# Optimization experiments

Measured on AMD Instinct MI355X. Metric: run time of the kernel, lower is better.

The kernel has to match this reference:

```python
import jax, jax.numpy as jnp
import numpy as np

B, NQ, NK = 4, 2048, 2048
DQ = DK = DV = 512
H = 8
DS = DV // H  # 64


def _layernorm(x, g, b, eps=1e-5):
    m = jnp.mean(x, axis=-1, keepdims=True)
    v = jnp.var(x, axis=-1, keepdims=True)
    return (x - m) * jax.lax.rsqrt(v + eps) * g + b


def setup_inputs() -> dict:
    key = jax.random.key(0)
    ks = jax.random.split(key, 16)
    def lin(k, fan_in, fan_out):
        # torch nn.Linear default init: U(-1/sqrt(fan_in), 1/sqrt(fan_in))
        bound = 1.0 / np.sqrt(fan_in)
        k1, k2 = jax.random.split(k)
        W = jax.random.uniform(k1, (fan_in, fan_out), jnp.float32, -bound, bound)
        b = jax.random.uniform(k2, (fan_out,), jnp.float32, -bound, bound)
        return W, b
    Wq, bq = lin(ks[0], DQ, DV)
    Wk, bk = lin(ks[1], DK, DV)
    Wv, bv = lin(ks[2], DK, DV)
    W0, b0 = lin(ks[3], DV, DV)
    W1, b1 = lin(ks[4], DV, DV)
    # xavier_uniform for kp/vp of shape (1, DS): bound = sqrt(6/(1+DS))
    xb = np.sqrt(6.0 / (1 + DS))
    kp = jax.random.uniform(ks[5], (DS,), jnp.float32, -xb, xb)
    vp = jax.random.uniform(ks[6], (DS,), jnp.float32, -xb, xb)
    return {
        "Q": jax.random.normal(ks[7], (B, NQ, DQ), jnp.float32),
        "K": jax.random.normal(ks[8], (B, NK, DK), jnp.float32),
        "Kpos": jax.random.uniform(ks[9], (B, NQ, NK), jnp.float32),
        "Wq": Wq, "bq": bq, "Wk": Wk, "bk": bk, "Wv": Wv, "bv": bv,
        "kp": kp, "vp": vp,
        "W0": W0, "b0": b0, "W1": W1, "b1": b1,
        "g0": jnp.ones((DV,), jnp.float32), "be0": jnp.zeros((DV,), jnp.float32),
        "g1": jnp.ones((DV,), jnp.float32), "be1": jnp.zeros((DV,), jnp.float32),
    }


def reference(Q, K, Kpos, Wq, bq, Wk, bk, Wv, bv, kp, vp, W0, b0, W1, b1, g0, be0, g1, be1):
    Qp = Q @ Wq + bq                       # [B,NQ,DV]
    Kp = K @ Wk + bk                       # [B,NK,DV]
    Vp = K @ Wv + bv                       # [B,NK,DV]
    # head split (torch split/cat along batch == reshape to [B,N,H,DS])
    Qh = Qp.reshape(B, NQ, H, DS)
    Kh = Kp.reshape(B, NK, H, DS)
    Vh = Vp.reshape(B, NK, H, DS)
    scale = 1.0 / np.sqrt(DV)              # NOTE: original scales by sqrt(dim_V), not per-head dim
    scores = jnp.einsum('bqhd,bkhd->bhqk', Qh, Kh) * scale
    # ShawRE key bias: KE[b,h,q,k] = Kpos[b,q,k] * <Qh[b,q,h,:], kp>
    qkp = jnp.einsum('bqhd,d->bhq', Qh, kp)          # [B,H,NQ]
    scores = scores + Kpos[:, None, :, :] * qkp[:, :, :, None]
    A = jax.nn.softmax(scores, axis=-1)              # [B,H,NQ,NK]
    out = jnp.einsum('bhqk,bkhd->bqhd', A, Vh)       # [B,NQ,H,DS]
    # ShawRE value bias: VE[b,q,h,:] = (sum_k A*Kpos) * vp
    akp = jnp.einsum('bhqk,bqk->bhq', A, Kpos)       # [B,H,NQ]
    out = out + akp.transpose(0, 2, 1)[..., None] * vp
    O = (Qh + out).reshape(B, NQ, DV)
    O = _layernorm(O, g0, be0)
    resO = O
    O = jax.nn.relu(O @ W0 + b0)           # fc_o[0] with relu (numlayers=2)
    O = resO + jax.nn.relu(O @ W1 + b1)    # fc_o[-1] + residual
    O = _layernorm(O, g1, be1)
    return O
```

## Files before the change

### kernel.cpp

```cpp
#include <hip/hip_runtime.h>
#include <math.h>

#define Bx  4
#define NQx 2048
#define NKx 2048
#define Dx  512
#define Hx  8

typedef __attribute__((ext_vector_type(8))) __bf16 bf16x8;
typedef __attribute__((ext_vector_type(4))) float f32x4;
typedef __attribute__((ext_vector_type(16))) float f32x16;

typedef const __attribute__((address_space(1))) unsigned int* gas_ptr;
typedef __attribute__((address_space(3))) unsigned int* lds_ptr;

__device__ __forceinline__ void gload16(const void* g, void* l){
  __builtin_amdgcn_global_load_lds((gas_ptr)g, (lds_ptr)l, 16, 0, 0);
}

__device__ __forceinline__ unsigned short f2bf(float f){
  union { float f; unsigned int u; } v; v.f = f;
  unsigned int r = (v.u + 0x7FFFu + ((v.u >> 16) & 1u)) >> 16;
  return (unsigned short)r;
}
__device__ __forceinline__ float bf2f(unsigned short u){
  union { unsigned int u; float f; } v; v.u = ((unsigned int)u) << 16; return v.f;
}
__device__ __forceinline__ unsigned int cvtpk_bf16(float a, float b){
  unsigned int d;
  asm("v_cvt_pk_bf16_f32 %0, %1, %2" : "=v"(d) : "v"(a), "v"(b));
  return d;
}
__device__ __forceinline__ void plane32_swap(unsigned int& a, unsigned int& b){
  asm("v_permlane32_swap_b32 %0, %1" : "+v"(a), "+v"(b));
}
__device__ __forceinline__ float fexp2(float x){
  float d; asm("v_exp_f32 %0, %1" : "=v"(d) : "v"(x)); return d;
}
__device__ __forceinline__ float fmax3(float a, float b, float c){
  float d; asm("v_max3_f32 %0, %1, %2, %3" : "=v"(d) : "v"(a), "v"(b), "v"(c)); return d;
}

__global__ __launch_bounds__(256) void mab_wt(
    const float* __restrict__ Wq, const float* __restrict__ Wk, const float* __restrict__ Wv,
    const float* __restrict__ W0, const float* __restrict__ W1,
    unsigned short* __restrict__ Wt)
{
  __shared__ unsigned short T[64][72];
  const int z = blockIdx.z;
  const float* W = (z==0)?Wq:(z==1)?Wk:(z==2)?Wv:(z==3)?W0:W1;
  unsigned short* O = Wt + (size_t)z*512*512;
  const int k0 = blockIdx.x*64, n0 = blockIdx.y*64;
  const int tid = threadIdx.x;
  #pragma unroll
  for (int i=0;i<4;++i){
    int id = tid + i*256;
    int r = id>>4, c4 = id&15;
    float4 v = *(const float4*)(W + (size_t)(k0+r)*512 + n0 + c4*4);
    ushort4 o; o.x=f2bf(v.x); o.y=f2bf(v.y); o.z=f2bf(v.z); o.w=f2bf(v.w);
    *(ushort4*)&T[r][c4*4] = o;
  }
  __syncthreads();
  #pragma unroll
  for (int i=0;i<2;++i){
    int id = tid + i*256;
    int c = id>>3, r8 = id&7;
    union { unsigned short u[8]; uint4 v; } o;
    #pragma unroll
    for (int j=0;j<8;++j) o.u[j] = T[r8*8+j][c];
    *(uint4*)(O + (size_t)(n0+c)*512 + k0 + r8*8) = o.v;
  }
}

__global__ __launch_bounds__(256) void mab_vt(
    const unsigned short* __restrict__ Vp, unsigned short* __restrict__ Vpt)
{
  __shared__ unsigned short T[64][72];
  const int r0 = blockIdx.x*64;
  const int c0 = blockIdx.y*64;
  const int b  = blockIdx.z;
  const int tid = threadIdx.x;
  #pragma unroll
  for (int i=0;i<2;++i){
    int id = tid + i*256;
    int r = id>>3, c8 = id&7;
    *(uint4*)&T[r][c8*8] = *(const uint4*)(Vp + (size_t)(b*NKx + r0+r)*512 + c0 + c8*8);
  }
  __syncthreads();
  #pragma unroll
  for (int i=0;i<2;++i){
    int id = tid + i*256;
    int c = id>>3, r8 = id&7;
    union { unsigned short u[8]; uint4 v; } o;
    #pragma unroll
    for (int j=0;j<8;++j) o.u[j] = T[r8*8+j][c];
    *(uint4*)(Vpt + ((size_t)(b*512) + c0 + c)*NKx + r0 + r8*8) = o.v;
  }
}

__global__ __launch_bounds__(256) void mab_gemm_proj(
    const float* __restrict__ Qf, const float* __restrict__ Kf,
    const unsigned short* __restrict__ Wt,
    const float* __restrict__ bq, const float* __restrict__ bk, const float* __restrict__ bv,
    unsigned short* __restrict__ Cb, float kscale)
{
  __shared__ unsigned short As[128][64];
  __shared__ unsigned short Bs[128][64];
  const int z = blockIdx.z;
  const float* A = (z==0) ? Qf : Kf;
  const unsigned short* W = Wt + (size_t)z*512*512;
  const float* bias = (z==0)?bq:((z==1)?bk:bv);
  const float sc = (z==1) ? kscale : 1.0f;
  const int m0 = blockIdx.y*128, n0 = blockIdx.x*128;
  const int tid = threadIdx.x, w = tid>>6, lane = tid&63, g = lane>>4, q16 = lane&15;
  const int wr = w>>1, wc = w&1;

  f32x4 acc[4][4];
  #pragma unroll
  for (int m=0;m<4;++m)
    #pragma unroll
    for (int n=0;n<4;++n) acc[m][n] = (f32x4){0.f,0.f,0.f,0.f};

  float4 areg[8];
  #pragma unroll
  for (int i=0;i<8;++i){
    int id = i*256 + tid, row = id>>4, qc = id&15;
    areg[i] = *(const float4*)(A + (size_t)(m0+row)*512 + qc*4);
  }

  for (int k0 = 0; k0 < 512; k0 += 64){
    __syncthreads();
    #pragma unroll
    for (int i=0;i<8;++i){
      int id = i*256 + tid, row = id>>4, qc = id&15;
      unsigned int lo = cvtpk_bf16(areg[i].x, areg[i].y);
      unsigned int hi = cvtpk_bf16(areg[i].z, areg[i].w);
      unsigned int* dst = (unsigned int*)((char*)&As[0][0] + row*128
                          + ((qc>>1) ^ (row&7))*16 + (qc&1)*8);
      dst[0] = lo; dst[1] = hi;
    }
    #pragma unroll
    for (int i=0;i<4;++i){
      int o   = (w*4 + i)*1024 + lane*16;
      int row = o >> 7;
      int c   = (o >> 4) & 7;
      int cs  = c ^ (row & 7);
      gload16(W + (size_t)(n0+row)*512 + k0 + cs*8, (char*)&Bs[0][0] + (w*4+i)*1024);
    }
    __syncthreads();
    if (k0 + 64 < 512){
      #pragma unroll
      for (int i=0;i<8;++i){
        int id = i*256 + tid, row = id>>4, qc = id&15;
        areg[i] = *(const float4*)(A + (size_t)(m0+row)*512 + (k0+64) + qc*4);
      }
    }
    #pragma unroll
    for (int ks=0;ks<2;++ks){
      bf16x8 af[4], bfr[4];
      #pragma unroll
      for (int m=0;m<4;++m){
        int row = wr*64 + m*16 + q16;
        int c   = (ks*4 + g) ^ (row & 7);
        af[m] = *(const bf16x8*)((const char*)&As[0][0] + row*128 + c*16);
      }
      #pragma unroll
      for (int n=0;n<4;++n){
        int row = wc*64 + n*16 + q16;
        int c   = (ks*4 + g) ^ (row & 7);
        bfr[n] = *(const bf16x8*)((const char*)&Bs[0][0] + row*128 + c*16);
      }
      #pragma unroll
      for (int m=0;m<4;++m)
        #pragma unroll
        for (int n=0;n<4;++n)
          acc[m][n] = __builtin_amdgcn_mfma_f32_16x16x32_bf16(af[m], bfr[n], acc[m][n], 0,0,0);
    }
  }

  const size_t ZS = (size_t)8192*512;
  #pragma unroll
  for (int m=0;m<4;++m){
    const int rowl = wr*64 + m*16 + g*4;
    #pragma unroll
    for (int n=0;n<4;++n){
      const int col = n0 + wc*64 + n*16 + q16;
      const float bv2 = bias[col];
      #pragma unroll
      for (int r=0;r<4;++r){
        float v = (acc[m][n][r] + bv2) * sc;
        Cb[(size_t)z*ZS + (size_t)(m0 + rowl + r)*512 + col] = f2bf(v);
      }
    }
  }
}

__global__ __launch_bounds__(256) void mab_gemm_mfma(
    const unsigned short* __restrict__ A, const unsigned short* __restrict__ W,
    const float* __restrict__ bias, const unsigned short* __restrict__ resb,
    unsigned short* __restrict__ Cb, float* __restrict__ Cf, int relu)
{
  __shared__ unsigned short As[128][64];
  __shared__ unsigned short Bs[128][64];
  const int m0 = blockIdx.y*128, n0 = blockIdx.x*128;
  const int tid = threadIdx.x, w = tid>>6, lane = tid&63, g = lane>>4, q16 = lane&15;
  const int wr = w>>1, wc = w&1;

  f32x4 acc[4][4];
  #pragma unroll
  for (int m=0;m<4;++m)
    #pragma unroll
    for (int n=0;n<4;++n) acc[m][n] = (f32x4){0.f,0.f,0.f,0.f};

  for (int k0 = 0; k0 < 512; k0 += 64){
    __syncthreads();
    #pragma unroll
    for (int i=0;i<4;++i){
      int o   = (w*4 + i)*1024 + lane*16;
      int row = o >> 7;
      int c   = (o >> 4) & 7;
      int cs  = c ^ (row & 7);
      gload16(A + (size_t)(m0+row)*512 + k0 + cs*8, (char*)&As[0][0] + (w*4+i)*1024);
      gload16(W + (size_t)(n0+row)*512 + k0 + cs*8, (char*)&Bs[0][0] + (w*4+i)*1024);
    }
    __syncthreads();
    #pragma unroll
    for (int ks=0;ks<2;++ks){
      bf16x8 af[4], bfr[4];
      #pragma unroll
      for (int m=0;m<4;++m){
        int row = wr*64 + m*16 + q16;
        int c   = (ks*4 + g) ^ (row & 7);
        af[m] = *(const bf16x8*)((const char*)&As[0][0] + row*128 + c*16);
      }
      #pragma unroll
      for (int n=0;n<4;++n){
        int row = wc*64 + n*16 + q16;
        int c   = (ks*4 + g) ^ (row & 7);
        bfr[n] = *(const bf16x8*)((const char*)&Bs[0][0] + row*128 + c*16);
      }
      #pragma unroll
      for (int m=0;m<4;++m)
        #pragma unroll
        for (int n=0;n<4;++n)
          acc[m][n] = __builtin_amdgcn_mfma_f32_16x16x32_bf16(af[m], bfr[n], acc[m][n], 0,0,0);
    }
  }

  #pragma unroll
  for (int m=0;m<4;++m){
    const int rowl = wr*64 + m*16 + g*4;
    #pragma unroll
    for (int n=0;n<4;++n){
      const int col = n0 + wc*64 + n*16 + q16;
      const float bv = bias[col];
      #pragma unroll
      for (int r=0;r<4;++r){
        float v = acc[m][n][r] + bv;
        if (relu) v = fmaxf(v, 0.f);
        size_t off = (size_t)(m0 + rowl + r)*512 + col;
        if (resb) v += bf2f(resb[off]);
        if (Cb) Cb[off] = f2bf(v);
        if (Cf) Cf[off] = v;
      }
    }
  }
}

__global__ __launch_bounds__(512, 2) void mab_attn7(
    const unsigned short* __restrict__ Qp, const unsigned short* __restrict__ Kp,
    const unsigned short* __restrict__ Vpt,
    const float* __restrict__ Kpos, const float* __restrict__ kp, const float* __restrict__ vp,
    float* __restrict__ X)
{
  __shared__ __align__(16) char pool[139264];

  const int qt = blockIdx.x;
  const int b  = blockIdx.y;
  const int q0 = qt*32;
  const int tid = threadIdx.x, w = tid>>6, lane = tid&63;
  const int q32 = lane & 31, hi = lane >> 5;
  const int h = w;

  char* Kbase = pool + w*8192;
  char* Vbase = pool + 65536 + w*8192;
  char* KQb   = pool + 131072;

  const unsigned short* Kg = Kp + ((size_t)b*NKx)*Dx + h*64;
  const unsigned short* Vg = Vpt + ((size_t)(b*512) + h*64)*NKx;
  const float* KPg = Kpos + (size_t)b*NQx*NKx + (size_t)q0*NKx;

  const int sr8 = lane>>3, sc8 = lane&7;
  const int sr4 = lane>>2, sc4 = lane&3;

  #pragma unroll
  for (int i=0;i<4;++i){
    int kr = i*8 + sr8, kcs = sc8 ^ (kr & 7);
    gload16(Kg + (size_t)kr*Dx + kcs*8, Kbase + i*1024);
    int vr = i*16 + sr4, vcs = sc4 ^ ((vr>>1) & 3);
    gload16(Vg + (size_t)vr*NKx + vcs*8, Vbase + i*1024);
  }
  if (w < 4){
    int pr = w*8 + sr8, pcs = sc8 ^ (pr & 7);
    gload16(KPg + (size_t)pr*NKx + pcs*4, KQb + w*1024);
  }

  const unsigned short* Qrowp = Qp + ((size_t)(b*NQx + q0 + q32))*Dx + h*64;
  bf16x8 qf[4];
  #pragma unroll
  for (int ds=0; ds<4; ++ds)
    qf[ds] = *(const bf16x8*)(Qrowp + ds*16 + hi*8);

  float qkp = 0.f;
  #pragma unroll
  for (int ds=0; ds<4; ++ds){
    union { bf16x8 v; unsigned short u[8]; } qa; qa.v = qf[ds];
    #pragma unroll
    for (int j=0;j<8;++j)
      qkp = fmaf(bf2f(qa.u[j]), kp[ds*16 + hi*8 + j], qkp);
  }
  qkp += __shfl_xor(qkp, 32);
  qkp *= 1.4426950408889634f;

  float m_i = -1e30f, l_i = 0.f, a_i = 0.f;
  f32x16 accT[2];
  #pragma unroll
  for (int db=0; db<2; ++db)
    #pragma unroll
    for (int r=0;r<16;++r) accT[db][r] = 0.f;

  __syncthreads();

  for (int t = 0; t < 64; ++t){
    const int cur = t & 1;
    const int k0 = t*32;

    if (t+1 < 64){
      const int k1 = k0 + 32;
      #pragma unroll
      for (int i=0;i<4;++i){
        int kr = i*8 + sr8, kcs = sc8 ^ (kr & 7);
        gload16(Kg + (size_t)(k1 + kr)*Dx + kcs*8, Kbase + (cur^1)*4096 + i*1024);
        int vr = i*16 + sr4, vcs = sc4 ^ ((vr>>1) & 3);
        gload16(Vg + (size_t)vr*NKx + k1 + vcs*8, Vbase + (cur^1)*4096 + i*1024);
      }
      if (w < 4){
        int pr = w*8 + sr8, pcs = sc8 ^ (pr & 7);
        gload16(KPg + (size_t)pr*NKx + k1 + pcs*4, KQb + (cur^1)*4096 + w*1024);
      }
    }
    __builtin_amdgcn_sched_barrier(0);

    f32x16 sT;
    #pragma unroll
    for (int r=0;r<16;++r) sT[r] = 0.f;
    __builtin_amdgcn_s_setprio(1);
    #pragma unroll
    for (int ds=0; ds<4; ++ds){
      int cc = (ds*2 + hi) ^ (q32 & 7);
      bf16x8 kf = *(const bf16x8*)(Kbase + cur*4096 + q32*128 + cc*16);
      sT = __builtin_amdgcn_mfma_f32_32x32x16_bf16(kf, qf[ds], sT, 0,0,0);
    }
    __builtin_amdgcn_s_setprio(0);

    f32x4 kq[4];
    #pragma unroll
    for (int a=0;a<4;++a){
      int cc = (a*2 + hi) ^ (q32 & 7);
      kq[a] = *(const f32x4*)(KQb + cur*4096 + q32*128 + cc*16);
    }

    #pragma unroll
    for (int r=0;r<16;++r)
      sT[r] = fmaf(kq[r>>2][r&3], qkp, sT[r]);

    float t0 = fmax3(sT[0],  sT[1],  sT[2]);
    float t1 = fmax3(sT[3],  sT[4],  sT[5]);
    float t2 = fmax3(sT[6],  sT[7],  sT[8]);
    float t3 = fmax3(sT[9],  sT[10], sT[11]);
    float t4 = fmax3(sT[12], sT[13], sT[14]);
    float rm = fmax3(fmax3(t0, t1, t2), fmax3(t3, t4, sT[15]), m_i);
    rm = fmaxf(rm, __shfl_xor(rm, 32));

    if (!__all(rm <= m_i + 11.544f)){
      float al = fexp2(m_i - rm);
      m_i = rm;
      l_i *= al; a_i *= al;
      #pragma unroll
      for (int db=0; db<2; ++db)
        #pragma unroll
        for (int r=0;r<16;++r) accT[db][r] *= al;
    }

    float psq[4] = {0.f,0.f,0.f,0.f};
    float pkq[4] = {0.f,0.f,0.f,0.f};
    #pragma unroll
    for (int r=0;r<16;++r){
      float p = fexp2(sT[r] - m_i);
      sT[r] = p;
      psq[r&3] += p;
      pkq[r&3] = fmaf(p, kq[r>>2][r&3], pkq[r&3]);
    }
    float ps = (psq[0]+psq[1]) + (psq[2]+psq[3]);
    float pk = (pkq[0]+pkq[1]) + (pkq[2]+pkq[3]);
    ps += __shfl_xor(ps, 32);
    pk += __shfl_xor(pk, 32);
    l_i += ps; a_i += pk;

    union PW { unsigned int u[4]; bf16x8 v; } pa[2];
    {
      unsigned int w0 = cvtpk_bf16(sT[0],  sT[1]);
      unsigned int w1 = cvtpk_bf16(sT[2],  sT[3]);
      unsigned int w2 = cvtpk_bf16(sT[4],  sT[5]);
      unsigned int w3 = cvtpk_bf16(sT[6],  sT[7]);
      unsigned int w4 = cvtpk_bf16(sT[8],  sT[9]);
      unsigned int w5 = cvtpk_bf16(sT[10], sT[11]);
      unsigned int w6 = cvtpk_bf16(sT[12], sT[13]);
      unsigned int w7 = cvtpk_bf16(sT[14], sT[15]);
      plane32_swap(w0, w2);
      plane32_swap(w1, w3);
      plane32_swap(w4, w6);
      plane32_swap(w5, w7);
      pa[0].u[0]=w0; pa[0].u[1]=w1; pa[0].u[2]=w2; pa[0].u[3]=w3;
      pa[1].u[0]=w4; pa[1].u[1]=w5; pa[1].u[2]=w6; pa[1].u[3]=w7;
    }

    __builtin_amdgcn_s_setprio(1);
    #pragma unroll
    for (int c2=0; c2<2; ++c2){
      #pragma unroll
      for (int db=0; db<2; ++db){
        int row = db*32 + q32;
        int cc  = (c2*2 + hi) ^ ((row>>1) & 3);
        bf16x8 vf = *(const bf16x8*)(Vbase + cur*4096 + row*64 + cc*16);
        accT[db] = __builtin_amdgcn_mfma_f32_32x32x16_bf16(vf, pa[c2].v, accT[db], 0,0,0);
      }
    }
    __builtin_amdgcn_s_setprio(0);

    __syncthreads();
  }

  float inv = 1.0f / l_i;
  float aw  = a_i * inv;
  float* Xrow = X + ((size_t)(b*NQx + q0 + q32))*Dx + h*64;
  #pragma unroll
  for (int db=0; db<2; ++db){
    #pragma unroll
    for (int a2=0; a2<4; ++a2){
      int d0 = db*32 + a2*8 + hi*4;
      f32x4 vpv = *(const f32x4*)(vp + d0);
      ushort4 qh = *(const ushort4*)(Qrowp + d0);
      float4 o;
      o.x = fmaf(accT[db][a2*4+0], inv, bf2f(qh.x) + aw*vpv[0]);
      o.y = fmaf(accT[db][a2*4+1], inv, bf2f(qh.y) + aw*vpv[1]);
      o.z = fmaf(accT[db][a2*4+2], inv, bf2f(qh.z) + aw*vpv[2]);
      o.w = fmaf(accT[db][a2*4+3], inv, bf2f(qh.w) + aw*vpv[3]);
      *(float4*)(Xrow + d0) = o;
    }
  }
}

__global__ __launch_bounds__(256) void mab_ln2(
    const float* __restrict__ Xin, const float* __restrict__ g,
    const float* __restrict__ be, float* __restrict__ Yf, unsigned short* __restrict__ Yb)
{
  const int row = blockIdx.x;
  const int tid = threadIdx.x;
  const float* x = Xin + (size_t)row*Dx;
  float2 v = *(const float2*)(x + tid*2);
  float s  = v.x + v.y;
  float sq = fmaf(v.x,v.x, v.y*v.y);
  #pragma unroll
  for (int m=1; m<64; m<<=1){ s += __shfl_xor(s,m); sq += __shfl_xor(sq,m); }
  __shared__ float red[2][4];
  const int wid = tid>>6, lane = tid&63;
  if (lane==0){ red[0][wid]=s; red[1][wid]=sq; }
  __syncthreads();
  s  = red[0][0]+red[0][1]+red[0][2]+red[0][3];
  sq = red[1][0]+red[1][1]+red[1][2]+red[1][3];
  float mean = s*(1.0f/Dx);
  float var  = sq*(1.0f/Dx) - mean*mean;
  float rstd = rsqrtf(var + 1e-5f);
  float2 gg = *(const float2*)(g  + tid*2);
  float2 bb = *(const float2*)(be + tid*2);
  float2 o;
  o.x = (v.x-mean)*rstd*gg.x + bb.x;
  o.y = (v.y-mean)*rstd*gg.y + bb.y;
  if (Yf) *(float2*)(Yf + (size_t)row*Dx + tid*2) = o;
  if (Yb){
    ushort2 ob; ob.x = f2bf(o.x); ob.y = f2bf(o.y);
    *(ushort2*)(Yb + (size_t)row*Dx + tid*2) = ob;
  }
}

extern "C" void kernel_launch(void* const* d_in, const int* in_sizes, int n_in,
                              void* d_out, int out_size, void* d_ws, size_t ws_size,
                              hipStream_t stream)
{
  const float* Q    = (const float*)d_in[0];
  const float* K    = (const float*)d_in[1];
  const float* Kpos = (const float*)d_in[2];
  const float* Wq   = (const float*)d_in[3];
  const float* bq   = (const float*)d_in[4];
  const float* Wk   = (const float*)d_in[5];
  const float* bk   = (const float*)d_in[6];
  const float* Wv   = (const float*)d_in[7];
  const float* bv   = (const float*)d_in[8];
  const float* kp   = (const float*)d_in[9];
  const float* vp   = (const float*)d_in[10];
  const float* W0   = (const float*)d_in[11];
  const float* b0   = (const float*)d_in[12];
  const float* W1   = (const float*)d_in[13];
  const float* b1   = (const float*)d_in[14];
  const float* g0   = (const float*)d_in[15];
  const float* be0  = (const float*)d_in[16];
  const float* g1   = (const float*)d_in[17];
  const float* be1  = (const float*)d_in[18];
  float* out = (float*)d_out;
  char* wsb  = (char*)d_ws;

  const size_t MB = 1024*1024;
  unsigned short* Qp  = (unsigned short*)(wsb);
  unsigned short* Kp  = (unsigned short*)(wsb + 8*MB);
  unsigned short* Vp  = (unsigned short*)(wsb + 16*MB);
  unsigned short* Vpt = (unsigned short*)(wsb + 24*MB);
  unsigned short* O0b = (unsigned short*)(wsb + 32*MB);
  unsigned short* Wt  = (unsigned short*)(wsb + 40*MB);
  unsigned short* T1  = Vp;

  const float kscale = 0.044194173824159216f * 1.4426950408889634f;

  mab_wt<<<dim3(8,8,5), 256, 0, stream>>>(Wq, Wk, Wv, W0, W1, Wt);
  mab_gemm_proj<<<dim3(4,64,3), 256, 0, stream>>>(Q, K, Wt, bq, bk, bv, Qp, kscale);
  mab_vt<<<dim3(32,8,4), 256, 0, stream>>>(Vp, Vpt);
  mab_attn7<<<dim3(64,4), 512, 0, stream>>>(Qp, Kp, Vpt, Kpos, kp, vp, out);
  mab_ln2<<<8192, 256, 0, stream>>>(out, g0, be0, nullptr, O0b);
  mab_gemm_mfma<<<dim3(4,64,1), 256, 0, stream>>>(
      O0b, Wt + (size_t)3*512*512, b0, nullptr, T1, nullptr, 1);
  mab_gemm_mfma<<<dim3(4,64,1), 256, 0, stream>>>(
      T1, Wt + (size_t)4*512*512, b1, O0b, nullptr, out, 1);
  mab_ln2<<<8192, 256, 0, stream>>>(out, g1, be1, out, nullptr);
}
```

Before: 207.2 us.

## Software-pipeline QK^T across tiles and fuse first LayerNorm into attention epilogue

The attention loop is restructured into a two-stage ping-pong: the QK^T MFMAs and the LDS fragment loads for the next key tile are issued before the softmax/PV work of the current tile, so matrix and vector work can overlap. The first LayerNorm is fused into the attention epilogue. Per-head partial sums are reduced through LDS across the 8 head waves, and normalized bf16 rows are written directly. This removes one kernel launch plus the fp32 write and reread of the intermediate tensor. In exchange it adds register pressure from the duplicate sT/kq/vf sets, which may hurt occupancy at 2 blocks per CU.

```diff
diff --git a/kernel.cpp b/kernel.cpp
--- a/kernel.cpp
+++ b/kernel.cpp
@@ -267,11 +267,12 @@
   }
 }
 
-__global__ __launch_bounds__(512, 2) void mab_attn7(
+__global__ __launch_bounds__(512, 2) void mab_attn8(
     const unsigned short* __restrict__ Qp, const unsigned short* __restrict__ Kp,
     const unsigned short* __restrict__ Vpt,
     const float* __restrict__ Kpos, const float* __restrict__ kp, const float* __restrict__ vp,
-    float* __restrict__ X)
+    const float* __restrict__ g0, const float* __restrict__ be0,
+    unsigned short* __restrict__ O0b)
 {
   __shared__ __align__(16) char pool[139264];
 
@@ -293,17 +294,38 @@
   const int sr8 = lane>>3, sc8 = lane&7;
   const int sr4 = lane>>2, sc4 = lane&3;
 
-  #pragma unroll
-  for (int i=0;i<4;++i){
-    int kr = i*8 + sr8, kcs = sc8 ^ (kr & 7);
-    gload16(Kg + (size_t)kr*Dx + kcs*8, Kbase + i*1024);
-    int vr = i*16 + sr4, vcs = sc4 ^ ((vr>>1) & 3);
-    gload16(Vg + (size_t)vr*NKx + vcs*8, Vbase + i*1024);
-  }
-  if (w < 4){
-    int pr = w*8 + sr8, pcs = sc8 ^ (pr & 7);
-    gload16(KPg + (size_t)pr*NKx + pcs*4, KQb + w*1024);
-  }
+  auto STAGE = [&](int t){
+    if (t >= 64) return;
+    const int buf = t & 1;
+    const int k1 = t*32;
+    #pragma unroll
+    for (int i=0;i<4;++i){
+      int kr = i*8 + sr8, kcs = sc8 ^ (kr & 7);
+      gload16(Kg + (size_t)(k1 + kr)*Dx + kcs*8, Kbase + buf*4096 + i*1024);
+      int vr = i*16 + sr4, vcs = sc4 ^ ((vr>>1) & 3);
+      gload16(Vg + (size_t)vr*NKx + k1 + vcs*8, Vbase + buf*4096 + i*1024);
+    }
+    if (w < 4){
+      int pr = w*8 + sr8, pcs = sc8 ^ (pr & 7);
+      gload16(KPg + (size_t)pr*NKx + k1 + pcs*4, KQb + buf*4096 + w*1024);
+    }
+  };
+
+  auto LOADREGS = [&](int buf, f32x4 (&kq)[4], bf16x8 (&vf)[2][2]){
+    #pragma unroll
+    for (int a=0;a<4;++a){
+      int cc = (a*2 + hi) ^ (q32 & 7);
+      kq[a] = *(const f32x4*)(KQb + buf*4096 + q32*128 + cc*16);
+    }
+    #pragma unroll
+    for (int c2=0;c2<2;++c2)
+      #pragma unroll
+      for (int db=0;db<2;++db){
+        int row = db*32 + q32;
+        int cc  = (c2*2 + hi) ^ ((row>>1) & 3);
+        vf[c2][db] = *(const bf16x8*)(Vbase + buf*4096 + row*64 + cc*16);
+      }
+  };
 
   const unsigned short* Qrowp = Qp + ((size_t)(b*NQx + q0 + q32))*Dx + h*64;
   bf16x8 qf[4];
@@ -311,6 +333,17 @@
   for (int ds=0; ds<4; ++ds)
     qf[ds] = *(const bf16x8*)(Qrowp + ds*16 + hi*8);
 
+  auto QKT = [&](int buf, f32x16& sT){
+    #pragma unroll
+    for (int r=0;r<16;++r) sT[r] = 0.f;
+    #pragma unroll
+    for (int ds=0; ds<4; ++ds){
+      int cc = (ds*2 + hi) ^ (q32 & 7);
+      bf16x8 kf = *(const bf16x8*)(Kbase + buf*4096 + q32*128 + cc*16);
+      sT = __builtin_amdgcn_mfma_f32_32x32x16_bf16(kf, qf[ds], sT, 0,0,0);
+    }
+  };
+
   float qkp = 0.f;
   #pragma unroll
   for (int ds=0; ds<4; ++ds){
@@ -329,51 +362,10 @@
     #pragma unroll
     for (int r=0;r<16;++r) accT[db][r] = 0.f;
 
-  __syncthreads();
-
-  for (int t = 0; t < 64; ++t){
-    const int cur = t & 1;
-    const int k0 = t*32;
-
-    if (t+1 < 64){
-      const int k1 = k0 + 32;
-      #pragma unroll
-      for (int i=0;i<4;++i){
-        int kr = i*8 + sr8, kcs = sc8 ^ (kr & 7);
-        gload16(Kg + (size_t)(k1 + kr)*Dx + kcs*8, Kbase + (cur^1)*4096 + i*1024);
-        int vr = i*16 + sr4, vcs = sc4 ^ ((vr>>1) & 3);
-        gload16(Vg + (size_t)vr*NKx + k1 + vcs*8, Vbase + (cur^1)*4096 + i*1024);
-      }
-      if (w < 4){
-        int pr = w*8 + sr8, pcs = sc8 ^ (pr & 7);
-        gload16(KPg + (size_t)pr*NKx + k1 + pcs*4, KQb + (cur^1)*4096 + w*1024);
-      }
-    }
-    __builtin_amdgcn_sched_barrier(0);
-
-    f32x16 sT;
-    #pragma unroll
-    for (int r=0;r<16;++r) sT[r] = 0.f;
-    __builtin_amdgcn_s_setprio(1);
-    #pragma unroll
-    for (int ds=0; ds<4; ++ds){
-      int cc = (ds*2 + hi) ^ (q32 & 7);
-      bf16x8 kf = *(const bf16x8*)(Kbase + cur*4096 + q32*128 + cc*16);
-      sT = __builtin_amdgcn_mfma_f32_32x32x16_bf16(kf, qf[ds], sT, 0,0,0);
-    }
-    __builtin_amdgcn_s_setprio(0);
-
-    f32x4 kq[4];
-    #pragma unroll
-    for (int a=0;a<4;++a){
-      int cc = (a*2 + hi) ^ (q32 & 7);
-      kq[a] = *(const f32x4*)(KQb + cur*4096 + q32*128 + cc*16);
-    }
-
+  auto FINISH = [&](f32x16& sT, f32x4 (&kq)[4], bf16x8 (&vf)[2][2]){
     #pragma unroll
     for (int r=0;r<16;++r)
       sT[r] = fmaf(kq[r>>2][r&3], qkp, sT[r]);
-
     float t0 = fmax3(sT[0],  sT[1],  sT[2]);
     float t1 = fmax3(sT[3],  sT[4],  sT[5]);
     float t2 = fmax3(sT[6],  sT[7],  sT[8]);
@@ -381,7 +373,6 @@
     float t4 = fmax3(sT[12], sT[13], sT[14]);
     float rm = fmax3(fmax3(t0, t1, t2), fmax3(t3, t4, sT[15]), m_i);
     rm = fmaxf(rm, __shfl_xor(rm, 32));
-
     if (!__all(rm <= m_i + 11.544f)){
       float al = fexp2(m_i - rm);
       m_i = rm;
@@ -391,7 +382,6 @@
         #pragma unroll
         for (int r=0;r<16;++r) accT[db][r] *= al;
     }
-
     float psq[4] = {0.f,0.f,0.f,0.f};
     float pkq[4] = {0.f,0.f,0.f,0.f};
     #pragma unroll
@@ -406,7 +396,6 @@
     ps += __shfl_xor(ps, 32);
     pk += __shfl_xor(pk, 32);
     l_i += ps; a_i += pk;
-
     union PW { unsigned int u[4]; bf16x8 v; } pa[2];
     {
       unsigned int w0 = cvtpk_bf16(sT[0],  sT[1]);
@@ -424,26 +413,49 @@
       pa[0].u[0]=w0; pa[0].u[1]=w1; pa[0].u[2]=w2; pa[0].u[3]=w3;
       pa[1].u[0]=w4; pa[1].u[1]=w5; pa[1].u[2]=w6; pa[1].u[3]=w7;
     }
-
     __builtin_amdgcn_s_setprio(1);
     #pragma unroll
     for (int c2=0; c2<2; ++c2){
       #pragma unroll
-      for (int db=0; db<2; ++db){
-        int row = db*32 + q32;
-        int cc  = (c2*2 + hi) ^ ((row>>1) & 3);
-        bf16x8 vf = *(const bf16x8*)(Vbase + cur*4096 + row*64 + cc*16);
-        accT[db] = __builtin_amdgcn_mfma_f32_32x32x16_bf16(vf, pa[c2].v, accT[db], 0,0,0);
-      }
+      for (int db=0; db<2; ++db)
+        accT[db] = __builtin_amdgcn_mfma_f32_32x32x16_bf16(vf[c2][db], pa[c2].v, accT[db], 0,0,0);
     }
     __builtin_amdgcn_s_setprio(0);
-
+  };
+
+  STAGE(0);
+  __syncthreads();
+
+  f32x16 sT0, sT1;
+  f32x4 kq0[4], kq1[4];
+  bf16x8 vf0[2][2], vf1[2][2];
+
+  STAGE(1);
+  __builtin_amdgcn_sched_barrier(0);
+  LOADREGS(0, kq0, vf0);
+  QKT(0, sT0);
+  __syncthreads();
+
+  for (int t = 1; t < 64; t += 2){
+    STAGE(t+1);
+    __builtin_amdgcn_sched_barrier(0);
+    LOADREGS(1, kq1, vf1);
+    QKT(1, sT1);
+    FINISH(sT0, kq0, vf0);
+    __syncthreads();
+    if (t+1 < 64){
+      STAGE(t+2);
+      __builtin_amdgcn_sched_barrier(0);
+      LOADREGS(0, kq0, vf0);
+      QKT(0, sT0);
+    }
+    FINISH(sT1, kq1, vf1);
     __syncthreads();
   }
 
   float inv = 1.0f / l_i;
   float aw  = a_i * inv;
-  float* Xrow = X + ((size_t)(b*NQx + q0 + q32))*Dx + h*64;
+  float s = 0.f, sq = 0.f;
   #pragma unroll
   for (int db=0; db<2; ++db){
     #pragma unroll
@@ -451,19 +463,56 @@
       int d0 = db*32 + a2*8 + hi*4;
       f32x4 vpv = *(const f32x4*)(vp + d0);
       ushort4 qh = *(const ushort4*)(Qrowp + d0);
-      float4 o;
-      o.x = fmaf(accT[db][a2*4+0], inv, bf2f(qh.x) + aw*vpv[0]);
-      o.y = fmaf(accT[db][a2*4+1], inv, bf2f(qh.y) + aw*vpv[1]);
-      o.z = fmaf(accT[db][a2*4+2], inv, bf2f(qh.z) + aw*vpv[2]);
-      o.w = fmaf(accT[db][a2*4+3], inv, bf2f(qh.w) + aw*vpv[3]);
-      *(float4*)(Xrow + d0) = o;
+      float o0 = fmaf(accT[db][a2*4+0], inv, bf2f(qh.x) + aw*vpv[0]);
+      float o1 = fmaf(accT[db][a2*4+1], inv, bf2f(qh.y) + aw*vpv[1]);
+      float o2 = fmaf(accT[db][a2*4+2], inv, bf2f(qh.z) + aw*vpv[2]);
+      float o3 = fmaf(accT[db][a2*4+3], inv, bf2f(qh.w) + aw*vpv[3]);
+      accT[db][a2*4+0]=o0; accT[db][a2*4+1]=o1;
+      accT[db][a2*4+2]=o2; accT[db][a2*4+3]=o3;
+      s += (o0+o1)+(o2+o3);
+      sq = fmaf(o0,o0, fmaf(o1,o1, fmaf(o2,o2, fmaf(o3,o3, sq))));
+    }
+  }
+  s  += __shfl_xor(s, 32);
+  sq += __shfl_xor(sq, 32);
+  float* lnred = (float*)pool;
+  if (hi == 0){
+    lnred[(q32*8 + w)*2 + 0] = s;
+    lnred[(q32*8 + w)*2 + 1] = sq;
+  }
+  __syncthreads();
+  float S = 0.f, SQ = 0.f;
+  #pragma unroll
+  for (int h2=0; h2<8; ++h2){
+    S  += lnred[(q32*8 + h2)*2 + 0];
+    SQ += lnred[(q32*8 + h2)*2 + 1];
+  }
+  float mean = S*(1.0f/512.0f);
+  float var  = SQ*(1.0f/512.0f) - mean*mean;
+  float rstd = rsqrtf(var + 1e-5f);
+  unsigned short* Orow = O0b + ((size_t)(b*NQx + q0 + q32))*Dx + h*64;
+  #pragma unroll
+  for (int db=0; db<2; ++db){
+    #pragma unroll
+    for (int a2=0; a2<4; ++a2){
+      int d0 = db*32 + a2*8 + hi*4;
+      f32x4 gg = *(const f32x4*)(g0  + h*64 + d0);
+      f32x4 bb = *(const f32x4*)(be0 + h*64 + d0);
+      float y0 = (accT[db][a2*4+0]-mean)*rstd*gg[0] + bb[0];
+      float y1 = (accT[db][a2*4+1]-mean)*rstd*gg[1] + bb[1];
+      float y2 = (accT[db][a2*4+2]-mean)*rstd*gg[2] + bb[2];
+      float y3 = (accT[db][a2*4+3]-mean)*rstd*gg[3] + bb[3];
+      uint2 pk2;
+      pk2.x = cvtpk_bf16(y0, y1);
+      pk2.y = cvtpk_bf16(y2, y3);
+      *(uint2*)(Orow + d0) = pk2;
     }
   }
 }
 
 __global__ __launch_bounds__(256) void mab_ln2(
     const float* __restrict__ Xin, const float* __restrict__ g,
-    const float* __restrict__ be, float* __restrict__ Yf, unsigned short* __restrict__ Yb)
+    const float* __restrict__ be, float* __restrict__ Yf)
 {
   const int row = blockIdx.x;
   const int tid = threadIdx.x;
@@ -487,11 +536,7 @@
   float2 o;
   o.x = (v.x-mean)*rstd*gg.x + bb.x;
   o.y = (v.y-mean)*rstd*gg.y + bb.y;
-  if (Yf) *(float2*)(Yf + (size_t)row*Dx + tid*2) = o;
-  if (Yb){
-    ushort2 ob; ob.x = f2bf(o.x); ob.y = f2bf(o.y);
-    *(ushort2*)(Yb + (size_t)row*Dx + tid*2) = ob;
-  }
+  *(float2*)(Yf + (size_t)row*Dx + tid*2) = o;
 }
 
 extern "C" void kernel_launch(void* const* d_in, const int* in_sizes, int n_in,
@@ -534,11 +579,10 @@
   mab_wt<<<dim3(8,8,5), 256, 0, stream>>>(Wq, Wk, Wv, W0, W1, Wt);
   mab_gemm_proj<<<dim3(4,64,3), 256, 0, stream>>>(Q, K, Wt, bq, bk, bv, Qp, kscale);
   mab_vt<<<dim3(32,8,4), 256, 0, stream>>>(Vp, Vpt);
-  mab_attn7<<<dim3(64,4), 512, 0, stream>>>(Qp, Kp, Vpt, Kpos, kp, vp, out);
-  mab_ln2<<<8192, 256, 0, stream>>>(out, g0, be0, nullptr, O0b);
+  mab_attn8<<<dim3(64,4), 512, 0, stream>>>(Qp, Kp, Vpt, Kpos, kp, vp, g0, be0, O0b);
   mab_gemm_mfma<<<dim3(4,64,1), 256, 0, stream>>>(
       O0b, Wt + (size_t)3*512*512, b0, nullptr, T1, nullptr, 1);
   mab_gemm_mfma<<<dim3(4,64,1), 256, 0, stream>>>(
       T1, Wt + (size_t)4*512*512, b1, O0b, nullptr, out, 1);
-  mab_ln2<<<8192, 256, 0, stream>>>(out, g1, be1, out, nullptr);
-}
+  mab_ln2<<<8192, 256, 0, stream>>>(out, g1, be1, out);
+}
```

New measurement: 196.1 us. 1.06x faster.
